# Performance work log

Measured on AMD Instinct MI355X. Metric: run time of the kernel, lower is better.

The kernel has to match this reference:

```python
import jax, jax.numpy as jnp
import numpy as np

B = 8
H_IN, W_IN = 448, 448
STRIDE = 32
NUM_CLASSES = 20
CONF_THRESH = 0.01
NMS_THRESH = 0.5
HS, WS = H_IN // STRIDE, W_IN // STRIDE  # 14, 14
N_CELLS = HS * WS  # 196
CHANNELS = [3, 64, 128, 256, 512, 512]
HEAD_OUT = 1 + NUM_CLASSES + 4  # 25


def _conv(x, w, stride):
    return jax.lax.conv_general_dilated(
        x, w, (stride, stride), 'SAME',
        dimension_numbers=('NCHW', 'OIHW', 'NCHW'))


def _create_grid():
    gy, gx = jnp.meshgrid(jnp.arange(HS), jnp.arange(WS), indexing='ij')
    return jnp.stack([gx, gy], -1).reshape(1, N_CELLS, 2).astype(jnp.float32)


def _iou_matrix(boxes):
    # boxes: [N,4] xyxy -> [N,N] pairwise IoU
    x1, y1, x2, y2 = boxes[:, 0], boxes[:, 1], boxes[:, 2], boxes[:, 3]
    area = jnp.maximum(x2 - x1, 0.0) * jnp.maximum(y2 - y1, 0.0)
    ix1 = jnp.maximum(x1[:, None], x1[None, :])
    iy1 = jnp.maximum(y1[:, None], y1[None, :])
    ix2 = jnp.minimum(x2[:, None], x2[None, :])
    iy2 = jnp.minimum(y2[:, None], y2[None, :])
    inter = jnp.maximum(ix2 - ix1, 0.0) * jnp.maximum(iy2 - iy1, 0.0)
    return inter / (area[:, None] + area[None, :] - inter + 1e-14)


def _nms_keep(scores, iou):
    # greedy per-class NMS; scores [N], iou [N,N] -> bool keep mask [N]
    order = jnp.argsort(-scores)
    iou_s = iou[order][:, order]
    idx = jnp.arange(N_CELLS)
    valid = scores[order] > CONF_THRESH

    def body(i, keep):
        sup = (iou_s[i] > NMS_THRESH) & (idx > i) & keep[i]
        return keep & (~sup)

    keep = jax.lax.fori_loop(0, N_CELLS, body, valid)
    return jnp.zeros(N_CELLS, bool).at[order].set(keep)


def setup_inputs() -> dict:
    key = jax.random.key(0)
    ks = jax.random.split(key, 8)
    x = jax.random.normal(ks[0], (B, 3, H_IN, W_IN), dtype=jnp.float32)
    params = {}
    for i in range(5):
        cin, cout = CHANNELS[i], CHANNELS[i + 1]
        std = np.sqrt(2.0 / (cin * 9))
        params[f'w{i+1}'] = jax.random.normal(ks[i + 1], (cout, cin, 3, 3), dtype=jnp.float32) * std
    std = np.sqrt(2.0 / CHANNELS[-1])
    params['w_head'] = jax.random.normal(ks[6], (HEAD_OUT, CHANNELS[-1], 1, 1), dtype=jnp.float32) * std
    return {'x': x, **params}


def reference(x, w1, w2, w3, w4, w5, w_head):
    # backbone: 5 stride-2 conv+relu stages -> stride 32
    h = x
    for w in (w1, w2, w3, w4, w5):
        h = jax.nn.relu(_conv(h, w, 2))
    pred = _conv(h, w_head, 1)                      # [B, 25, 14, 14]
    pred = pred.reshape(B, HEAD_OUT, N_CELLS).transpose(0, 2, 1)  # [B, N, 25]

    conf = jax.nn.sigmoid(pred[..., 0:1])                              # [B,N,1]
    cls_scores = jax.nn.softmax(pred[..., 1:1 + NUM_CLASSES], -1) * conf  # [B,N,C]
    txtytwth = pred[..., 1 + NUM_CLASSES:]                             # [B,N,4]

    grid = _create_grid()                                              # [1,N,2]
    xy = (jax.nn.sigmoid(txtytwth[..., :2]) + grid) * STRIDE
    wh = jnp.exp(txtytwth[..., 2:]) * STRIDE
    scale = jnp.array([W_IN, H_IN, W_IN, H_IN], dtype=jnp.float32)
    boxes = jnp.concatenate([xy - wh * 0.5, xy + wh * 0.5], -1) / scale
    boxes = jnp.clip(boxes, 0.0, 1.0)                                  # [B,N,4]

    iou = jax.vmap(_iou_matrix)(boxes)                                 # [B,N,N]
    # per-class NMS, vmapped over classes then batch
    nms_c = jax.vmap(_nms_keep, in_axes=(-1, None), out_axes=-1)       # [N,C]
    keep = jax.vmap(nms_c, in_axes=(0, 0))(cls_scores, iou)            # [B,N,C]
    final_scores = cls_scores * keep
    return jnp.concatenate([boxes, final_scores], -1)                  # [B,N,4+C]
```

## Files before the change

kernel.cpp:

```cpp
#include <hip/hip_runtime.h>
#include <math.h>

#define BATCH 8
#define NCELLS 196
#define NCLS 20
#define HEADC 25

typedef __attribute__((ext_vector_type(8))) short short8;
typedef __attribute__((ext_vector_type(4))) float f32x4;
#define MFMA16(a,b,c) __builtin_amdgcn_mfma_f32_16x16x32_bf16(a,b,c,0,0,0)

__device__ __forceinline__ unsigned short f2bf(float x) {
    union { float f; unsigned u; } a; a.f = x;
    unsigned r = a.u + 0x7FFFu + ((a.u >> 16) & 1u);
    return (unsigned short)(r >> 16);
}
__device__ __forceinline__ float bf2f(unsigned short h) {
    union { unsigned u; float f; } a; a.u = ((unsigned)h) << 16;
    return a.f;
}
__device__ __forceinline__ void split_bf(float x, unsigned short& h, unsigned short& l) {
    h = f2bf(x);
    l = f2bf(x - bf2f(h));
}

template<int CIN, int COUT>
__global__ void prep_w(const float* __restrict__ w, unsigned short* __restrict__ whi,
                       unsigned short* __restrict__ wlo) {
    constexpr int G = COUT / 16, CH = CIN / 32;
    int idx = blockIdx.x * 256 + threadIdx.x;
    if (idx >= 9 * CIN * COUT) return;
    int j    = idx & 7;
    int lane = (idx >> 3) & 63;
    int fg   = idx >> 9;
    int g    = fg % G;
    int fc   = fg / G;
    int chunk = fc % CH;
    int plane = fc / CH;
    int m = lane & 15, quad = lane >> 4;
    int co = g * 16 + m;
    int ci = chunk * 32 + quad * 8 + j;
    int ky = plane / 3, kx = plane % 3;
    float v = w[((co * CIN + ci) * 3 + ky) * 3 + kx];
    unsigned short h, l; split_bf(v, h, l);
    whi[idx] = h; wlo[idx] = l;
}

__global__ void conv1_kernel(const float* __restrict__ x, const float* __restrict__ w1,
                             unsigned short* __restrict__ ohi, unsigned short* __restrict__ olo) {
    __shared__ float sW[27][64];
    __shared__ float sX[3][3][66];
    int bid = blockIdx.x;
    int xseg = bid % 7;  bid /= 7;
    int oy   = bid % 224;
    int b    = bid / 224;
    int ox0  = xseg * 32;

    for (int e = threadIdx.x; e < 1728; e += 256) {
        int k = e >> 6, co = e & 63;
        sW[k][co] = w1[co * 27 + k];
    }
    for (int e = threadIdx.x; e < 594; e += 256) {
        int ci = e / 198;
        int r  = e - ci * 198;
        int ky = r / 66;
        int lx = r - ky * 66;
        int iy = 2 * oy + ky;
        int ix = 2 * ox0 + lx;
        float v = 0.f;
        if (lx < 65 && iy < 448 && ix < 448)
            v = x[(((size_t)b * 3 + ci) * 448 + iy) * 448 + ix];
        sX[ci][ky][lx] = v;
    }
    __syncthreads();

    int pxl = threadIdx.x >> 3;
    int cog = threadIdx.x & 7;
    float acc[8] = {0.f,0.f,0.f,0.f,0.f,0.f,0.f,0.f};
    #pragma unroll
    for (int ci = 0; ci < 3; ci++) {
        #pragma unroll
        for (int ky = 0; ky < 3; ky++) {
            const float* row = sX[ci][ky];
            #pragma unroll
            for (int kx = 0; kx < 3; kx++) {
                float iv = row[2 * pxl + kx];
                int k = (ci * 3 + ky) * 3 + kx;
                float4 wa = *(const float4*)&sW[k][cog * 8];
                float4 wb = *(const float4*)&sW[k][cog * 8 + 4];
                acc[0] += wa.x * iv; acc[1] += wa.y * iv; acc[2] += wa.z * iv; acc[3] += wa.w * iv;
                acc[4] += wb.x * iv; acc[5] += wb.y * iv; acc[6] += wb.z * iv; acc[7] += wb.w * iv;
            }
        }
    }
    union { unsigned short u[8]; uint4 v; } ph, pl;
    #pragma unroll
    for (int u = 0; u < 8; u++) {
        float v = fmaxf(acc[u], 0.f);
        split_bf(v, ph.u[u], pl.u[u]);
    }
    size_t base = ((size_t)(b * 224 + oy) * 224 + ox0 + pxl) * 64 + cog * 8;
    *(uint4*)&ohi[base] = ph.v;
    *(uint4*)&olo[base] = pl.v;
}

template<int CIN, int COUT, int HIN, int WIN, int KSPLIT, bool PARTIAL>
__launch_bounds__(256, 4)
__global__ void conv_mfma(const unsigned short* __restrict__ ahi, const unsigned short* __restrict__ alo,
                          const unsigned short* __restrict__ whi, const unsigned short* __restrict__ wlo,
                          unsigned short* __restrict__ ohi, unsigned short* __restrict__ olo,
                          float* __restrict__ part) {
    constexpr int HOUT = HIN / 2, WOUT = WIN / 2;
    constexpr int TX = (WOUT + 7) / 8, TY = (HOUT + 7) / 8;
    constexpr int COG = COUT / 128;
    constexpr int CH_TOT = CIN / 32;
    constexpr int CH = CH_TOT / KSPLIT;
    constexpr int G = COUT / 16;
    constexpr int PLANE_E = 17 * 17 * 32;
    constexpr size_t PSZ = (size_t)BATCH * HOUT * WOUT * COUT;

    __shared__ __align__(16) unsigned short sA[2 * PLANE_E];

    int bid = blockIdx.x;
    int ks  = bid % KSPLIT; bid /= KSPLIT;
    int txi = bid % TX;     bid /= TX;
    int tyi = bid % TY;     bid /= TY;
    int cg  = bid % COG;
    int b   = bid / COG;
    int oy0 = tyi * 8, ox0 = txi * 8;
    int iy0 = oy0 * 2, ix0 = ox0 * 2;

    int tid = threadIdx.x;
    int w   = tid >> 6;
    int lane = tid & 63;
    int n = lane & 15, quad = lane >> 4;

    int oyl[4], oxl[4], pbase[4];
    #pragma unroll
    for (int nt = 0; nt < 4; nt++) {
        int oyq = nt >> 1, oxq = nt & 1;
        int oy_off = oyq * 4 + (n >> 2);
        int ox_off = oxq * 4 + (n & 3);
        oyl[nt] = oy0 + oy_off;
        oxl[nt] = ox0 + ox_off;
        pbase[nt] = 2 * oy_off * 17 + 2 * ox_off;
    }

    f32x4 zero = {0.f, 0.f, 0.f, 0.f};
    f32x4 acc[2][4];
    #pragma unroll
    for (int ct = 0; ct < 2; ct++)
        #pragma unroll
        for (int nt = 0; nt < 4; nt++) acc[ct][nt] = zero;

    int g0 = cg * 8 + w * 2;

    for (int ch = 0; ch < CH; ch++) {
        int chunk = ks * CH + ch;
        int ci0 = chunk * 32;
        __syncthreads();
        for (int e = tid; e < 17 * 17 * 8; e += 256) {
            int pxi = e >> 3, grp = e & 7;
            int liy = pxi / 17, lix = pxi - liy * 17;
            int iy = iy0 + liy, ix = ix0 + lix;
            uint4 v = make_uint4(0u, 0u, 0u, 0u);
            if (iy < HIN && ix < WIN) {
                const unsigned short* src = ((grp & 4) ? alo : ahi)
                    + ((size_t)(b * HIN + iy) * WIN + ix) * CIN + ci0 + (grp & 3) * 8;
                v = *(const uint4*)src;
            }
            int u = pxi * 4 + ((grp & 3) ^ ((pxi >> 1) & 3));
            *(uint4*)&sA[((grp >> 2) ? PLANE_E : 0) + u * 8] = v;
        }
        __syncthreads();
        #pragma unroll
        for (int pl = 0; pl < 9; pl++) {
            int ky = pl / 3, kx = pl % 3;
            size_t fbase = ((size_t)(pl * CH_TOT + chunk) * G + g0) * 512 + lane * 8;
            short8 Ah0 = *(const short8*)(whi + fbase);
            short8 Ah1 = *(const short8*)(whi + fbase + 512);
            short8 Al0 = *(const short8*)(wlo + fbase);
            short8 Al1 = *(const short8*)(wlo + fbase + 512);
            int dp = ky * 17 + kx;
            #pragma unroll
            for (int nt = 0; nt < 4; nt++) {
                int p = pbase[nt] + dp;
                int u = p * 4 + (quad ^ ((p >> 1) & 3));
                short8 Bh = *(const short8*)&sA[u * 8];
                short8 Bl = *(const short8*)&sA[PLANE_E + u * 8];
                acc[0][nt] = MFMA16(Ah0, Bh, acc[0][nt]);
                acc[0][nt] = MFMA16(Ah0, Bl, acc[0][nt]);
                acc[0][nt] = MFMA16(Al0, Bh, acc[0][nt]);
                acc[1][nt] = MFMA16(Ah1, Bh, acc[1][nt]);
                acc[1][nt] = MFMA16(Ah1, Bl, acc[1][nt]);
                acc[1][nt] = MFMA16(Al1, Bh, acc[1][nt]);
            }
        }
    }
    int cob = cg * 128 + w * 32;
    #pragma unroll
    for (int ct = 0; ct < 2; ct++) {
        #pragma unroll
        for (int nt = 0; nt < 4; nt++) {
            if (oyl[nt] >= HOUT || oxl[nt] >= WOUT) continue;
            size_t base = ((size_t)(b * HOUT + oyl[nt]) * WOUT + oxl[nt]) * COUT
                          + cob + ct * 16 + quad * 4;
            if (PARTIAL) {
                *(f32x4*)&part[(size_t)ks * PSZ + base] = acc[ct][nt];
            } else {
                unsigned long long h64 = 0ull, l64 = 0ull;
                #pragma unroll
                for (int r = 0; r < 4; r++) {
                    float v = fmaxf(acc[ct][nt][r], 0.f);
                    unsigned short hh, ll; split_bf(v, hh, ll);
                    h64 |= ((unsigned long long)hh) << (16 * r);
                    l64 |= ((unsigned long long)ll) << (16 * r);
                }
                *(unsigned long long*)&ohi[base] = h64;
                *(unsigned long long*)&olo[base] = l64;
            }
        }
    }
}

template<int KS>
__global__ void reduceN_split(const float* __restrict__ p, unsigned short* __restrict__ oh,
                              unsigned short* __restrict__ ol, int n) {
    int n4 = n >> 2;
    int i = blockIdx.x * 256 + threadIdx.x;
    if (i >= n4) return;
    const float4* p4 = (const float4*)p;
    float4 s = p4[i];
    #pragma unroll
    for (int k = 1; k < KS; k++) {
        float4 t = p4[i + (size_t)k * n4];
        s.x += t.x; s.y += t.y; s.z += t.z; s.w += t.w;
    }
    float v[4] = { fmaxf(s.x,0.f), fmaxf(s.y,0.f), fmaxf(s.z,0.f), fmaxf(s.w,0.f) };
    unsigned long long h64 = 0ull, l64 = 0ull;
    #pragma unroll
    for (int r = 0; r < 4; r++) {
        unsigned short hh, ll; split_bf(v[r], hh, ll);
        h64 |= ((unsigned long long)hh) << (16 * r);
        l64 |= ((unsigned long long)ll) << (16 * r);
    }
    *(unsigned long long*)&oh[i * 4] = h64;
    *(unsigned long long*)&ol[i * 4] = l64;
}

__global__ void head_kernel(const unsigned short* __restrict__ ah, const unsigned short* __restrict__ al,
                            const float* __restrict__ wh, float* __restrict__ pred) {
    int wave = threadIdx.x >> 6;
    int lane = threadIdx.x & 63;
    int cellid = blockIdx.x * 4 + wave;
    float acc[HEADC];
    #pragma unroll
    for (int c = 0; c < HEADC; c++) acc[c] = 0.f;
    for (int it = 0; it < 8; it++) {
        int ci = it * 64 + lane;
        size_t idx = (size_t)cellid * 512 + ci;
        float a = bf2f(ah[idx]) + bf2f(al[idx]);
        #pragma unroll
        for (int c = 0; c < HEADC; c++) acc[c] += a * wh[c * 512 + ci];
    }
    #pragma unroll
    for (int c = 0; c < HEADC; c++) {
        float v = acc[c];
        v += __shfl_down(v, 32); v += __shfl_down(v, 16); v += __shfl_down(v, 8);
        v += __shfl_down(v, 4);  v += __shfl_down(v, 2);  v += __shfl_down(v, 1);
        if (lane == 0) pred[(size_t)cellid * HEADC + c] = v;
    }
}

__global__ void decode_kernel(const float* __restrict__ pred, float* __restrict__ out,
                              float* __restrict__ cls) {
    int i = blockIdx.x * 256 + threadIdx.x;
    if (i >= BATCH * NCELLS) return;
    const float* p = pred + (size_t)i * HEADC;
    int cell = i % NCELLS;
    int gx = cell % 14, gy = cell / 14;
    float conf = 1.f / (1.f + expf(-p[0]));
    float m = p[1];
    #pragma unroll
    for (int c = 1; c < NCLS; c++) m = fmaxf(m, p[1 + c]);
    float e[NCLS], s = 0.f;
    #pragma unroll
    for (int c = 0; c < NCLS; c++) { e[c] = expf(p[1 + c] - m); s += e[c]; }
    float inv = conf / s;
    #pragma unroll
    for (int c = 0; c < NCLS; c++) cls[(size_t)i * NCLS + c] = e[c] * inv;
    float cx = (1.f / (1.f + expf(-p[21])) + gx) * 32.f;
    float cy = (1.f / (1.f + expf(-p[22])) + gy) * 32.f;
    float w  = expf(p[23]) * 32.f;
    float h  = expf(p[24]) * 32.f;
    float x1 = (cx - 0.5f * w) / 448.f, y1 = (cy - 0.5f * h) / 448.f;
    float x2 = (cx + 0.5f * w) / 448.f, y2 = (cy + 0.5f * h) / 448.f;
    x1 = fminf(fmaxf(x1, 0.f), 1.f); y1 = fminf(fmaxf(y1, 0.f), 1.f);
    x2 = fminf(fmaxf(x2, 0.f), 1.f); y2 = fminf(fmaxf(y2, 0.f), 1.f);
    float* o = out + (size_t)i * 24;
    o[0] = x1; o[1] = y1; o[2] = x2; o[3] = y2;
}

__global__ void iou_kernel(const float* __restrict__ out, float* __restrict__ iou) {
    int idx = blockIdx.x * 256 + threadIdx.x;
    if (idx >= BATCH * NCELLS * NCELLS) return;
    int j = idx % NCELLS;
    int i = (idx / NCELLS) % NCELLS;
    int b = idx / (NCELLS * NCELLS);
    const float* bi = out + (((size_t)b * NCELLS) + i) * 24;
    const float* bj = out + (((size_t)b * NCELLS) + j) * 24;
    float ai = fmaxf(bi[2] - bi[0], 0.f) * fmaxf(bi[3] - bi[1], 0.f);
    float aj = fmaxf(bj[2] - bj[0], 0.f) * fmaxf(bj[3] - bj[1], 0.f);
    float ix1 = fmaxf(bi[0], bj[0]), iy1 = fmaxf(bi[1], bj[1]);
    float ix2 = fminf(bi[2], bj[2]), iy2 = fminf(bi[3], bj[3]);
    float inter = fmaxf(ix2 - ix1, 0.f) * fmaxf(iy2 - iy1, 0.f);
    iou[idx] = inter / (ai + aj - inter + 1e-14f);
}

__global__ void nms_kernel(const float* __restrict__ cls, const float* __restrict__ iou,
                           float* __restrict__ out) {
    int b = blockIdx.x / NCLS;
    int c = blockIdx.x % NCLS;
    __shared__ float sc[NCELLS];
    __shared__ float ssort[NCELLS];
    __shared__ int   ord[NCELLS];
    __shared__ __align__(16) unsigned long long smask[NCELLS][4];
    int j = threadIdx.x;
    int lane = j & 63;
    int w = j >> 6;
    float sj = 0.f;
    if (j < NCELLS) {
        sj = cls[(((size_t)b * NCELLS) + j) * NCLS + c];
        sc[j] = sj;
    }
    __syncthreads();
    if (j < NCELLS) {
        int r = 0;
        for (int k = 0; k < NCELLS; k++) {
            float sk = sc[k];
            r += (sk > sj) || (sk == sj && k < j);
        }
        ord[r] = j; ssort[r] = sj;
    }
    __syncthreads();
    const float* iob = iou + (size_t)b * NCELLS * NCELLS;
    int oc[4];
    #pragma unroll
    for (int k = 0; k < 4; k++) {
        int cidx = k * 64 + lane;
        oc[k] = (cidx < NCELLS) ? ord[cidx] : 0;
    }
    for (int i = w; i < NCELLS; i += 4) {
        const float* rowp = iob + ord[i] * NCELLS;
        #pragma unroll
        for (int k = 0; k < 4; k++) {
            int cidx = k * 64 + lane;
            bool sup = false;
            if (cidx < NCELLS && cidx > i)
                sup = rowp[oc[k]] > 0.5f;
            unsigned long long m = __ballot(sup);
            if (lane == 0) smask[i][k] = m;
        }
    }
    __syncthreads();
    unsigned long long keep[4];
    #pragma unroll
    for (int k = 0; k < 4; k++) {
        int cidx = k * 64 + lane;
        bool valid = (cidx < NCELLS) && (ssort[cidx] > 0.01f);
        keep[k] = __ballot(valid);
    }
    #pragma unroll
    for (int wi = 0; wi < 4; wi++) {
        int base = wi * 64;
        int lim = (NCELLS - base < 64) ? (NCELLS - base) : 64;
        for (int t = 0; t < lim; t++) {
            if ((keep[wi] >> t) & 1ull) {
                int i = base + t;
                keep[0] &= ~smask[i][0];
                keep[1] &= ~smask[i][1];
                keep[2] &= ~smask[i][2];
                keep[3] &= ~smask[i][3];
            }
        }
    }
    if (j < NCELLS) {
        bool kept = (keep[w] >> lane) & 1ull;
        out[(((size_t)b * NCELLS) + ord[j]) * 24 + 4 + c] = kept ? ssort[j] : 0.f;
    }
}

extern "C" void kernel_launch(void* const* d_in, const int* in_sizes, int n_in,
                              void* d_out, int out_size, void* d_ws, size_t ws_size,
                              hipStream_t stream) {
    const float* x  = (const float*)d_in[0];
    const float* w1 = (const float*)d_in[1];
    const float* w2 = (const float*)d_in[2];
    const float* w3 = (const float*)d_in[3];
    const float* w4 = (const float*)d_in[4];
    const float* w5 = (const float*)d_in[5];
    const float* wh = (const float*)d_in[6];
    float* out = (float*)d_out;
    char* base = (char*)d_ws;

    unsigned short* a1h = (unsigned short*)(base);
    unsigned short* a1l = a1h + 25690112;
    unsigned short* a3h = (unsigned short*)(base);
    unsigned short* a3l = a3h + 6422528;
    float* part4 = (float*)(base + 25690112);
    float* part5 = (float*)(base);
    unsigned short* a5h = (unsigned short*)(base + 51380224);
    unsigned short* a5l = a5h + 802816;
    float* pred = (float*)(base + 54589440);
    float* clsb = (float*)(base + 54746240);
    float* ioub = (float*)(base + 54871680);
    unsigned short* a2h = (unsigned short*)(base + 102760448);
    unsigned short* a2l = a2h + 12845056;
    unsigned short* a4h = (unsigned short*)(base + 102760448);
    unsigned short* a4l = a4h + 3211264;
    unsigned short* w2h = (unsigned short*)(base + 154140672);
    unsigned short* w3h = w2h + 73728;
    unsigned short* w4h = w3h + 294912;
    unsigned short* w5h = w4h + 1179648;
    unsigned short* w2l = (unsigned short*)(base + 161955840);
    unsigned short* w3l = w2l + 73728;
    unsigned short* w4l = w3l + 294912;
    unsigned short* w5l = w4l + 1179648;

    prep_w<64, 128> <<<288,  256, 0, stream>>>(w2, w2h, w2l);
    prep_w<128, 256><<<1152, 256, 0, stream>>>(w3, w3h, w3l);
    prep_w<256, 512><<<4608, 256, 0, stream>>>(w4, w4h, w4l);
    prep_w<512, 512><<<9216, 256, 0, stream>>>(w5, w5h, w5l);

    conv1_kernel<<<12544, 256, 0, stream>>>(x, w1, a1h, a1l);

    conv_mfma<64, 128, 224, 224, 1, false><<<1568, 256, 0, stream>>>(
        a1h, a1l, w2h, w2l, a2h, a2l, nullptr);
    conv_mfma<128, 256, 112, 112, 1, false><<<784, 256, 0, stream>>>(
        a2h, a2l, w3h, w3l, a3h, a3l, nullptr);
    conv_mfma<256, 512, 56, 56, 2, true><<<1024, 256, 0, stream>>>(
        a3h, a3l, w4h, w4l, nullptr, nullptr, part4);
    reduceN_split<2><<<3136, 256, 0, stream>>>(part4, a4h, a4l, 3211264);
    conv_mfma<512, 512, 28, 28, 8, true><<<1024, 256, 0, stream>>>(
        a4h, a4l, w5h, w5l, nullptr, nullptr, part5);
    reduceN_split<8><<<784, 256, 0, stream>>>(part5, a5h, a5l, 802816);

    head_kernel<<<392, 256, 0, stream>>>(a5h, a5l, wh, pred);
    decode_kernel<<<7, 256, 0, stream>>>(pred, out, clsb);
    iou_kernel<<<1201, 256, 0, stream>>>(out, ioub);
    nms_kernel<<<160, 256, 0, stream>>>(clsb, ioub, out);
}
```

Baseline: 445.6 us.

## Retile conv MFMA waves, merge weight prep kernels, fuse head with decode

```diff
diff --git a/kernel.cpp b/kernel.cpp
--- a/kernel.cpp
+++ b/kernel.cpp
@@ -24,12 +24,10 @@
     l = f2bf(x - bf2f(h));
 }
 
-template<int CIN, int COUT>
-__global__ void prep_w(const float* __restrict__ w, unsigned short* __restrict__ whi,
-                       unsigned short* __restrict__ wlo) {
-    constexpr int G = COUT / 16, CH = CIN / 32;
-    int idx = blockIdx.x * 256 + threadIdx.x;
-    if (idx >= 9 * CIN * COUT) return;
+__device__ __forceinline__ void prep_one(const float* __restrict__ w, int CIN, int COUT,
+                                         int idx, unsigned short* __restrict__ whi,
+                                         unsigned short* __restrict__ wlo) {
+    int G = COUT >> 4, CH = CIN >> 5;
     int j    = idx & 7;
     int lane = (idx >> 3) & 63;
     int fg   = idx >> 9;
@@ -37,13 +35,28 @@
     int fc   = fg / G;
     int chunk = fc % CH;
     int plane = fc / CH;
-    int m = lane & 15, quad = lane >> 4;
-    int co = g * 16 + m;
-    int ci = chunk * 32 + quad * 8 + j;
+    int co = g * 16 + (lane & 15);
+    int ci = chunk * 32 + (lane >> 4) * 8 + j;
     int ky = plane / 3, kx = plane % 3;
     float v = w[((co * CIN + ci) * 3 + ky) * 3 + kx];
     unsigned short h, l; split_bf(v, h, l);
     whi[idx] = h; wlo[idx] = l;
+}
+__global__ void prep_all(const float* __restrict__ w2, const float* __restrict__ w3,
+                         const float* __restrict__ w4, const float* __restrict__ w5,
+                         unsigned short* __restrict__ w2h, unsigned short* __restrict__ w2l,
+                         unsigned short* __restrict__ w3h, unsigned short* __restrict__ w3l,
+                         unsigned short* __restrict__ w4h, unsigned short* __restrict__ w4l,
+                         unsigned short* __restrict__ w5h, unsigned short* __restrict__ w5l) {
+    int idx = blockIdx.x * 256 + threadIdx.x;
+    const int n2 = 73728, n3 = 294912, n4 = 1179648, n5 = 2359296;
+    if (idx < n2) { prep_one(w2, 64, 128, idx, w2h, w2l); return; }
+    idx -= n2;
+    if (idx < n3) { prep_one(w3, 128, 256, idx, w3h, w3l); return; }
+    idx -= n3;
+    if (idx < n4) { prep_one(w4, 256, 512, idx, w4h, w4l); return; }
+    idx -= n4;
+    if (idx < n5) { prep_one(w5, 512, 512, idx, w5h, w5l); }
 }
 
 __global__ void conv1_kernel(const float* __restrict__ x, const float* __restrict__ w1,
@@ -134,26 +147,28 @@
     int w   = tid >> 6;
     int lane = tid & 63;
     int n = lane & 15, quad = lane >> 4;
-
-    int oyl[4], oxl[4], pbase[4];
-    #pragma unroll
-    for (int nt = 0; nt < 4; nt++) {
-        int oyq = nt >> 1, oxq = nt & 1;
-        int oy_off = oyq * 4 + (n >> 2);
-        int ox_off = oxq * 4 + (n & 3);
-        oyl[nt] = oy0 + oy_off;
-        oxl[nt] = ox0 + ox_off;
-        pbase[nt] = 2 * oy_off * 17 + 2 * ox_off;
+    int cohalf = w & 1;
+    int pxhalf = w >> 1;
+
+    int oyl[2], oxl[2], pbase[2];
+    #pragma unroll
+    for (int t = 0; t < 2; t++) {
+        int nt = pxhalf * 2 + t;
+        int oy_off = (nt >> 1) * 4 + (n >> 2);
+        int ox_off = (nt & 1) * 4 + (n & 3);
+        oyl[t] = oy0 + oy_off;
+        oxl[t] = ox0 + ox_off;
+        pbase[t] = 2 * oy_off * 17 + 2 * ox_off;
     }
 
     f32x4 zero = {0.f, 0.f, 0.f, 0.f};
-    f32x4 acc[2][4];
-    #pragma unroll
-    for (int ct = 0; ct < 2; ct++)
-        #pragma unroll
-        for (int nt = 0; nt < 4; nt++) acc[ct][nt] = zero;
-
-    int g0 = cg * 8 + w * 2;
+    f32x4 acc[4][2];
+    #pragma unroll
+    for (int g = 0; g < 4; g++)
+        #pragma unroll
+        for (int t = 0; t < 2; t++) acc[g][t] = zero;
+
+    int g0 = cg * 8 + cohalf * 4;
 
     for (int ch = 0; ch < CH; ch++) {
         int chunk = ks * CH + ch;
@@ -177,41 +192,47 @@
         for (int pl = 0; pl < 9; pl++) {
             int ky = pl / 3, kx = pl % 3;
             size_t fbase = ((size_t)(pl * CH_TOT + chunk) * G + g0) * 512 + lane * 8;
-            short8 Ah0 = *(const short8*)(whi + fbase);
-            short8 Ah1 = *(const short8*)(whi + fbase + 512);
-            short8 Al0 = *(const short8*)(wlo + fbase);
-            short8 Al1 = *(const short8*)(wlo + fbase + 512);
+            short8 Ah[4], Al[4];
+            #pragma unroll
+            for (int g = 0; g < 4; g++) {
+                Ah[g] = *(const short8*)(whi + fbase + (size_t)g * 512);
+                Al[g] = *(const short8*)(wlo + fbase + (size_t)g * 512);
+            }
             int dp = ky * 17 + kx;
+            short8 Bh[2], Bl[2];
             #pragma unroll
-            for (int nt = 0; nt < 4; nt++) {
-                int p = pbase[nt] + dp;
+            for (int t = 0; t < 2; t++) {
+                int p = pbase[t] + dp;
                 int u = p * 4 + (quad ^ ((p >> 1) & 3));
-                short8 Bh = *(const short8*)&sA[u * 8];
-                short8 Bl = *(const short8*)&sA[PLANE_E + u * 8];
-                acc[0][nt] = MFMA16(Ah0, Bh, acc[0][nt]);
-                acc[0][nt] = MFMA16(Ah0, Bl, acc[0][nt]);
-                acc[0][nt] = MFMA16(Al0, Bh, acc[0][nt]);
-                acc[1][nt] = MFMA16(Ah1, Bh, acc[1][nt]);
-                acc[1][nt] = MFMA16(Ah1, Bl, acc[1][nt]);
-                acc[1][nt] = MFMA16(Al1, Bh, acc[1][nt]);
-            }
-        }
-    }
-    int cob = cg * 128 + w * 32;
-    #pragma unroll
-    for (int ct = 0; ct < 2; ct++) {
-        #pragma unroll
-        for (int nt = 0; nt < 4; nt++) {
-            if (oyl[nt] >= HOUT || oxl[nt] >= WOUT) continue;
-            size_t base = ((size_t)(b * HOUT + oyl[nt]) * WOUT + oxl[nt]) * COUT
-                          + cob + ct * 16 + quad * 4;
+                Bh[t] = *(const short8*)&sA[u * 8];
+                Bl[t] = *(const short8*)&sA[PLANE_E + u * 8];
+            }
+            #pragma unroll
+            for (int g = 0; g < 4; g++) {
+                #pragma unroll
+                for (int t = 0; t < 2; t++) {
+                    acc[g][t] = MFMA16(Ah[g], Bh[t], acc[g][t]);
+                    acc[g][t] = MFMA16(Ah[g], Bl[t], acc[g][t]);
+                    acc[g][t] = MFMA16(Al[g], Bh[t], acc[g][t]);
+                }
+            }
+        }
+    }
+    int cob = cg * 128 + cohalf * 64;
+    #pragma unroll
+    for (int g = 0; g < 4; g++) {
+        #pragma unroll
+        for (int t = 0; t < 2; t++) {
+            if (oyl[t] >= HOUT || oxl[t] >= WOUT) continue;
+            size_t base = ((size_t)(b * HOUT + oyl[t]) * WOUT + oxl[t]) * COUT
+                          + cob + g * 16 + quad * 4;
             if (PARTIAL) {
-                *(f32x4*)&part[(size_t)ks * PSZ + base] = acc[ct][nt];
+                *(f32x4*)&part[(size_t)ks * PSZ + base] = acc[g][t];
             } else {
                 unsigned long long h64 = 0ull, l64 = 0ull;
                 #pragma unroll
                 for (int r = 0; r < 4; r++) {
-                    float v = fmaxf(acc[ct][nt][r], 0.f);
+                    float v = fmaxf(acc[g][t][r], 0.f);
                     unsigned short hh, ll; split_bf(v, hh, ll);
                     h64 |= ((unsigned long long)hh) << (16 * r);
                     l64 |= ((unsigned long long)ll) << (16 * r);
@@ -248,8 +269,10 @@
     *(unsigned long long*)&ol[i * 4] = l64;
 }
 
-__global__ void head_kernel(const unsigned short* __restrict__ ah, const unsigned short* __restrict__ al,
-                            const float* __restrict__ wh, float* __restrict__ pred) {
+__global__ void head_decode_kernel(const unsigned short* __restrict__ ah,
+                                   const unsigned short* __restrict__ al,
+                                   const float* __restrict__ wh,
+                                   float* __restrict__ out, float* __restrict__ cls) {
     int wave = threadIdx.x >> 6;
     int lane = threadIdx.x & 63;
     int cellid = blockIdx.x * 4 + wave;
@@ -268,37 +291,32 @@
         float v = acc[c];
         v += __shfl_down(v, 32); v += __shfl_down(v, 16); v += __shfl_down(v, 8);
         v += __shfl_down(v, 4);  v += __shfl_down(v, 2);  v += __shfl_down(v, 1);
-        if (lane == 0) pred[(size_t)cellid * HEADC + c] = v;
-    }
-}
-
-__global__ void decode_kernel(const float* __restrict__ pred, float* __restrict__ out,
-                              float* __restrict__ cls) {
-    int i = blockIdx.x * 256 + threadIdx.x;
-    if (i >= BATCH * NCELLS) return;
-    const float* p = pred + (size_t)i * HEADC;
-    int cell = i % NCELLS;
-    int gx = cell % 14, gy = cell / 14;
-    float conf = 1.f / (1.f + expf(-p[0]));
-    float m = p[1];
-    #pragma unroll
-    for (int c = 1; c < NCLS; c++) m = fmaxf(m, p[1 + c]);
-    float e[NCLS], s = 0.f;
-    #pragma unroll
-    for (int c = 0; c < NCLS; c++) { e[c] = expf(p[1 + c] - m); s += e[c]; }
-    float inv = conf / s;
-    #pragma unroll
-    for (int c = 0; c < NCLS; c++) cls[(size_t)i * NCLS + c] = e[c] * inv;
-    float cx = (1.f / (1.f + expf(-p[21])) + gx) * 32.f;
-    float cy = (1.f / (1.f + expf(-p[22])) + gy) * 32.f;
-    float w  = expf(p[23]) * 32.f;
-    float h  = expf(p[24]) * 32.f;
-    float x1 = (cx - 0.5f * w) / 448.f, y1 = (cy - 0.5f * h) / 448.f;
-    float x2 = (cx + 0.5f * w) / 448.f, y2 = (cy + 0.5f * h) / 448.f;
-    x1 = fminf(fmaxf(x1, 0.f), 1.f); y1 = fminf(fmaxf(y1, 0.f), 1.f);
-    x2 = fminf(fmaxf(x2, 0.f), 1.f); y2 = fminf(fmaxf(y2, 0.f), 1.f);
-    float* o = out + (size_t)i * 24;
-    o[0] = x1; o[1] = y1; o[2] = x2; o[3] = y2;
+        acc[c] = v;
+    }
+    if (lane == 0) {
+        int cell = cellid % NCELLS;
+        int gx = cell % 14, gy = cell / 14;
+        float conf = 1.f / (1.f + expf(-acc[0]));
+        float m = acc[1];
+        #pragma unroll
+        for (int c = 1; c < NCLS; c++) m = fmaxf(m, acc[1 + c]);
+        float e[NCLS], s = 0.f;
+        #pragma unroll
+        for (int c = 0; c < NCLS; c++) { e[c] = expf(acc[1 + c] - m); s += e[c]; }
+        float inv = conf / s;
+        #pragma unroll
+        for (int c = 0; c < NCLS; c++) cls[(size_t)cellid * NCLS + c] = e[c] * inv;
+        float cx = (1.f / (1.f + expf(-acc[21])) + gx) * 32.f;
+        float cy = (1.f / (1.f + expf(-acc[22])) + gy) * 32.f;
+        float bw = expf(acc[23]) * 32.f;
+        float bh = expf(acc[24]) * 32.f;
+        float x1 = (cx - 0.5f * bw) / 448.f, y1 = (cy - 0.5f * bh) / 448.f;
+        float x2 = (cx + 0.5f * bw) / 448.f, y2 = (cy + 0.5f * bh) / 448.f;
+        x1 = fminf(fmaxf(x1, 0.f), 1.f); y1 = fminf(fmaxf(y1, 0.f), 1.f);
+        x2 = fminf(fmaxf(x2, 0.f), 1.f); y2 = fminf(fmaxf(y2, 0.f), 1.f);
+        float* o = out + (size_t)cellid * 24;
+        o[0] = x1; o[1] = y1; o[2] = x2; o[3] = y2;
+    }
 }
 
 __global__ void iou_kernel(const float* __restrict__ out, float* __restrict__ iou) {
@@ -411,7 +429,6 @@
     float* part5 = (float*)(base);
     unsigned short* a5h = (unsigned short*)(base + 51380224);
     unsigned short* a5l = a5h + 802816;
-    float* pred = (float*)(base + 54589440);
     float* clsb = (float*)(base + 54746240);
     float* ioub = (float*)(base + 54871680);
     unsigned short* a2h = (unsigned short*)(base + 102760448);
@@ -427,10 +444,8 @@
     unsigned short* w4l = w3l + 294912;
     unsigned short* w5l = w4l + 1179648;
 
-    prep_w<64, 128> <<<288,  256, 0, stream>>>(w2, w2h, w2l);
-    prep_w<128, 256><<<1152, 256, 0, stream>>>(w3, w3h, w3l);
-    prep_w<256, 512><<<4608, 256, 0, stream>>>(w4, w4h, w4l);
-    prep_w<512, 512><<<9216, 256, 0, stream>>>(w5, w5h, w5l);
+    prep_all<<<15264, 256, 0, stream>>>(w2, w3, w4, w5,
+                                        w2h, w2l, w3h, w3l, w4h, w4l, w5h, w5l);
 
     conv1_kernel<<<12544, 256, 0, stream>>>(x, w1, a1h, a1l);
 
@@ -445,8 +460,7 @@
         a4h, a4l, w5h, w5l, nullptr, nullptr, part5);
     reduceN_split<8><<<784, 256, 0, stream>>>(part5, a5h, a5l, 802816);
 
-    head_kernel<<<392, 256, 0, stream>>>(a5h, a5l, wh, pred);
-    decode_kernel<<<7, 256, 0, stream>>>(pred, out, clsb);
+    head_decode_kernel<<<392, 256, 0, stream>>>(a5h, a5l, wh, out, clsb);
     iou_kernel<<<1201, 256, 0, stream>>>(out, ioub);
     nms_kernel<<<160, 256, 0, stream>>>(clsb, ioub, out);
 }
```

New measurement: 464.2 us. +4.2%, slower.
